# Kernel tuning notes

Measured on AMD Instinct MI355X. Metric: run time of the kernel, lower is better.

The kernel has to match this reference:

```python
import jax, jax.numpy as jnp
import numpy as np

N_NODES = 50000
N_EDGES = 800000
HIDDEN = 128
N_GRAPHS = 256
N_CLASSES = 10


def setup_inputs() -> dict:
    key = jax.random.key(0)
    ks = jax.random.split(key, 9)
    x = jax.random.normal(ks[0], (N_NODES, HIDDEN), dtype=jnp.float32)
    edge_index = jax.random.randint(ks[1], (2, N_EDGES), 0, N_NODES, dtype=jnp.int64)
    batch = jnp.sort(jax.random.randint(ks[2], (N_NODES,), 0, N_GRAPHS, dtype=jnp.int64))
    s = 1.0 / np.sqrt(HIDDEN)
    W1 = jax.random.uniform(ks[3], (HIDDEN, HIDDEN), jnp.float32, -s, s)
    b1 = jax.random.uniform(ks[4], (HIDDEN,), jnp.float32, -s, s)
    W2 = jax.random.uniform(ks[5], (HIDDEN, HIDDEN), jnp.float32, -s, s)
    b2 = jax.random.uniform(ks[6], (HIDDEN,), jnp.float32, -s, s)
    Wl = jax.random.uniform(ks[7], (HIDDEN, N_CLASSES), jnp.float32, -s, s)
    bl = jax.random.uniform(ks[8], (N_CLASSES,), jnp.float32, -s, s)
    return {"x": x, "edge_index": edge_index, "batch": batch,
            "W1": W1, "b1": b1, "W2": W2, "b2": b2, "Wl": Wl, "bl": bl}


def _gin_conv(x, src, dst, W1, b1, W2, b2):
    # GINConv, eps=0: nn(x + sum_{j->i} x_j); messages flow src -> dst
    agg = jax.ops.segment_sum(x[src], dst, num_segments=N_NODES)
    h = x + agg
    h = jnp.maximum(h @ W1 + b1, 0.0) @ W2 + b2  # shared 2-layer MLP
    return h


def reference(x, edge_index, batch, W1, b1, W2, b2, Wl, bl):
    src, dst = edge_index[0], edge_index[1]
    h = jnp.maximum(_gin_conv(x, src, dst, W1, b1, W2, b2), 0.0)
    h = jnp.maximum(_gin_conv(h, src, dst, W1, b1, W2, b2), 0.0)
    h = _gin_conv(h, src, dst, W1, b1, W2, b2)
    # global mean pool over graphs
    sums = jax.ops.segment_sum(h, batch, num_segments=N_GRAPHS)
    cnt = jax.ops.segment_sum(jnp.ones((N_NODES,), h.dtype), batch, num_segments=N_GRAPHS)
    pooled = sums / jnp.maximum(cnt, 1.0)[:, None]
    # dropout is identity in eval mode
    return pooled @ Wl + bl
```

## Files before the change

kernel.cpp:

```cpp
#include <hip/hip_runtime.h>

#define N_NODES  50000
#define N_EDGES  800000
#define HIDDEN   128
#define N_GRAPHS 256
#define N_CLASSES 10
#define WLD 136

typedef short short8 __attribute__((ext_vector_type(8)));
typedef float floatx4 __attribute__((ext_vector_type(4)));

__device__ inline unsigned short bf16_rtne(float x) {
    unsigned u = __float_as_uint(x);
    unsigned r = ((u >> 16) & 1u) + 0x7fffu;
    return (unsigned short)((u + r) >> 16);
}

__global__ void prep_kernel(const int* __restrict__ dst, int* __restrict__ deg, int* __restrict__ epos,
                            const float* __restrict__ W1, unsigned short* __restrict__ W1b,
                            const float* __restrict__ W2, unsigned short* __restrict__ W2b,
                            const float4* __restrict__ X, uint4* __restrict__ Xb,
                            int* __restrict__ counter) {
    int b = blockIdx.x;
    if (b < 3125) {
        int e = b * 256 + threadIdx.x;
        epos[e] = atomicAdd(&deg[dst[e]], 1);
    } else if (b < 3253) {
        int idx = (b - 3125) * 256 + threadIdx.x;
        if (idx == 0) counter[0] = 0;
        int which = idx >> 14, sub = idx & (HIDDEN * HIDDEN - 1);
        int k = sub >> 7, n = sub & 127;
        (which ? W2b : W1b)[n * HIDDEN + k] = bf16_rtne((which ? W2 : W1)[sub]);
    } else {
        int i = (b - 3253) * 256 + threadIdx.x;
        int n = i >> 4, c = i & 15;
        float4 a = X[(size_t)n * 32 + c * 2], v = X[(size_t)n * 32 + c * 2 + 1];
        uint4 o;
        o.x = (unsigned)bf16_rtne(a.x) | ((unsigned)bf16_rtne(a.y) << 16);
        o.y = (unsigned)bf16_rtne(a.z) | ((unsigned)bf16_rtne(a.w) << 16);
        o.z = (unsigned)bf16_rtne(v.x) | ((unsigned)bf16_rtne(v.y) << 16);
        o.w = (unsigned)bf16_rtne(v.z) | ((unsigned)bf16_rtne(v.w) << 16);
        Xb[(size_t)(c >> 2) * N_NODES * 4 + (size_t)n * 4 + (c & 3)] = o;
    }
}

__global__ void offsets_kernel(const int* __restrict__ deg, int* __restrict__ row_start,
                               int* __restrict__ counter) {
    int n = blockIdx.x * blockDim.x + threadIdx.x;
    int d = (n < N_NODES) ? deg[n] : 0;
    int lane = threadIdx.x & 63;
    int incl = d;
    #pragma unroll
    for (int off = 1; off < 64; off <<= 1) {
        int v = __shfl_up(incl, off, 64);
        if (lane >= off) incl += v;
    }
    int excl = incl - d;
    int total = __shfl(incl, 63, 64);
    int base = 0;
    if (lane == 0) base = atomicAdd(counter, total);
    base = __shfl(base, 0, 64);
    if (n < N_NODES) row_start[n] = base + excl;
}

__global__ void place_kernel(const int* __restrict__ src, const int* __restrict__ dst,
                             const int* __restrict__ epos, const int* __restrict__ row_start,
                             int* __restrict__ csr_src) {
    int e = blockIdx.x * blockDim.x + threadIdx.x;
    if (e >= N_EDGES) return;
    csr_src[row_start[dst[e]] + epos[e]] = src[e];
}

__device__ inline void acc_bf2(unsigned d, float& f0, float& f1) {
    f0 += __uint_as_float(d << 16);
    f1 += __uint_as_float(d & 0xffff0000u);
}
__device__ inline void acc8(const uint4 v, float* a) {
    acc_bf2(v.x, a[0], a[1]); acc_bf2(v.y, a[2], a[3]);
    acc_bf2(v.z, a[4], a[5]); acc_bf2(v.w, a[6], a[7]);
}

__global__ void agg_kernel(const uint4* __restrict__ Xb, const int* __restrict__ row_start,
                           const int* __restrict__ deg, const int* __restrict__ csr_src,
                           uint4* __restrict__ Tb ) {
    int s = blockIdx.x & 3;
    int n = (blockIdx.x >> 2) * 64 + (threadIdx.x >> 2);
    int chunk = threadIdx.x & 3;
    if (n >= N_NODES) return;
    const uint4* Ts = Xb + (size_t)s * (N_NODES * 4);
    float a[8];
    #pragma unroll
    for (int j = 0; j < 8; ++j) a[j] = 0.f;
    {
        uint4 v = Ts[(size_t)n * 4 + chunk];
        acc8(v, a);
    }
    int rs = row_start[n], d = deg[n];
    int i = 0;
    for (; i + 8 <= d; i += 8) {
        int s0 = csr_src[rs + i + 0];
        int s1 = csr_src[rs + i + 1];
        int s2 = csr_src[rs + i + 2];
        int s3 = csr_src[rs + i + 3];
        int s4 = csr_src[rs + i + 4];
        int s5 = csr_src[rs + i + 5];
        int s6 = csr_src[rs + i + 6];
        int s7 = csr_src[rs + i + 7];
        uint4 v0 = Ts[(size_t)s0 * 4 + chunk];
        uint4 v1 = Ts[(size_t)s1 * 4 + chunk];
        uint4 v2 = Ts[(size_t)s2 * 4 + chunk];
        uint4 v3 = Ts[(size_t)s3 * 4 + chunk];
        uint4 v4 = Ts[(size_t)s4 * 4 + chunk];
        uint4 v5 = Ts[(size_t)s5 * 4 + chunk];
        uint4 v6 = Ts[(size_t)s6 * 4 + chunk];
        uint4 v7 = Ts[(size_t)s7 * 4 + chunk];
        acc8(v0, a); acc8(v1, a); acc8(v2, a); acc8(v3, a);
        acc8(v4, a); acc8(v5, a); acc8(v6, a); acc8(v7, a);
    }
    for (; i + 2 <= d; i += 2) {
        int s0 = csr_src[rs + i + 0];
        int s1 = csr_src[rs + i + 1];
        uint4 v0 = Ts[(size_t)s0 * 4 + chunk];
        uint4 v1 = Ts[(size_t)s1 * 4 + chunk];
        acc8(v0, a); acc8(v1, a);
    }
    if (i < d) {
        int s0 = csr_src[rs + i];
        uint4 v0 = Ts[(size_t)s0 * 4 + chunk];
        acc8(v0, a);
    }
    uint4 o;
    o.x = (unsigned)bf16_rtne(a[0]) | ((unsigned)bf16_rtne(a[1]) << 16);
    o.y = (unsigned)bf16_rtne(a[2]) | ((unsigned)bf16_rtne(a[3]) << 16);
    o.z = (unsigned)bf16_rtne(a[4]) | ((unsigned)bf16_rtne(a[5]) << 16);
    o.w = (unsigned)bf16_rtne(a[6]) | ((unsigned)bf16_rtne(a[7]) << 16);
    Tb[(size_t)n * 16 + s * 4 + chunk] = o;
}

__global__ __launch_bounds__(256)
void mm_mfma(const unsigned short* __restrict__ Ab,
             const unsigned short* __restrict__ Bw,
             const float* __restrict__ bias,
             unsigned short* __restrict__ Cb, int relu, int blocked) {
    __shared__ unsigned short WhS[64 * WLD];

    int t = threadIdx.x;
    int col_base = blockIdx.y * 64;
    {
        const short8* gh = (const short8*)(Bw + (size_t)col_base * HIDDEN);
        #pragma unroll
        for (int i = 0; i < 4; ++i) {
            int idx = i * 256 + t;
            int row = idx >> 4, kk = (idx & 15) * 8;
            *(short8*)(WhS + row * WLD + kk) = gh[idx];
        }
    }
    __syncthreads();

    int w = t >> 6;
    int l = t & 63;
    int lane16 = l & 15;
    int quad = l >> 4;
    int row_base = blockIdx.x * 128 + w * 32;

    floatx4 acc[2][4];
    #pragma unroll
    for (int m = 0; m < 2; ++m)
        #pragma unroll
        for (int nt = 0; nt < 4; ++nt) acc[m][nt] = (floatx4){0.f, 0.f, 0.f, 0.f};

    #pragma unroll
    for (int kc = 0; kc < 4; ++kc) {
        int k0 = kc * 32 + quad * 8;
        short8 af[2];
        #pragma unroll
        for (int m = 0; m < 2; ++m) {
            int r = row_base + m * 16 + lane16;
            if (r < N_NODES) af[m] = *(const short8*)(Ab + (size_t)r * HIDDEN + k0);
            else             af[m] = (short8){0,0,0,0,0,0,0,0};
        }
        short8 bh[4];
        #pragma unroll
        for (int nt = 0; nt < 4; ++nt)
            bh[nt] = *(const short8*)(WhS + (nt * 16 + lane16) * WLD + k0);
        #pragma unroll
        for (int m = 0; m < 2; ++m)
            #pragma unroll
            for (int nt = 0; nt < 4; ++nt)
                acc[m][nt] = __builtin_amdgcn_mfma_f32_16x16x32_bf16(af[m], bh[nt], acc[m][nt], 0, 0, 0);
    }
    #pragma unroll
    for (int nt = 0; nt < 4; ++nt) {
        int col = col_base + nt * 16 + lane16;
        float b = bias[col];
        #pragma unroll
        for (int m = 0; m < 2; ++m) {
            #pragma unroll
            for (int reg = 0; reg < 4; ++reg) {
                int r = row_base + m * 16 + quad * 4 + reg;
                if (r < N_NODES) {
                    float o = acc[m][nt][reg] + b;
                    if (relu) o = fmaxf(o, 0.f);
                    size_t oi = blocked
                        ? ((size_t)(col >> 5) * N_NODES + r) * 32 + (col & 31)
                        : (size_t)r * HIDDEN + col;
                    Cb[oi] = bf16_rtne(o);
                }
            }
        }
    }
}

__global__ void pool_head_kernel(const unsigned short* __restrict__ H, const int* __restrict__ batch,
                                 const float* __restrict__ Wl, const float* __restrict__ bl,
                                 float* __restrict__ out) {
    int g = blockIdx.x;
    int t = threadIdx.x;
    __shared__ int bounds[2];
    __shared__ float acc2[2 * HIDDEN];
    __shared__ float mean[HIDDEN];

    if (t < 2) {
        int target = g + t;
        int lo = 0, hi = N_NODES;
        while (lo < hi) {
            int mid = (lo + hi) >> 1;
            if (batch[mid] < target) lo = mid + 1; else hi = mid;
        }
        bounds[t] = lo;
    }
    __syncthreads();
    int r0 = bounds[0], r1 = bounds[1];

    int c = t & 127, half = t >> 7;
    float s = 0.f;
    for (int r = r0 + half; r < r1; r += 2)
        s += __uint_as_float((unsigned)H[(size_t)r * HIDDEN + c] << 16);
    acc2[half * HIDDEN + c] = s;
    __syncthreads();
    if (t < HIDDEN) {
        float cntf = (float)(r1 - r0);
        mean[t] = (acc2[t] + acc2[HIDDEN + t]) / fmaxf(cntf, 1.0f);
    }
    __syncthreads();
    if (t < N_CLASSES) {
        float o = bl[t];
        #pragma unroll 8
        for (int k = 0; k < HIDDEN; ++k) o = fmaf(mean[k], Wl[k * N_CLASSES + t], o);
        out[(size_t)g * N_CLASSES + t] = o;
    }
}

extern "C" void kernel_launch(void* const* d_in, const int* in_sizes, int n_in,
                              void* d_out, int out_size, void* d_ws, size_t ws_size,
                              hipStream_t stream) {
    const float* x   = (const float*)d_in[0];
    const int*   ei  = (const int*)d_in[1];
    const int*   bat = (const int*)d_in[2];
    const float* W1  = (const float*)d_in[3];
    const float* b1  = (const float*)d_in[4];
    const float* W2  = (const float*)d_in[5];
    const float* b2  = (const float*)d_in[6];
    const float* Wl  = (const float*)d_in[7];
    const float* bl  = (const float*)d_in[8];
    float* out = (float*)d_out;

    const int* src = ei;
    const int* dst = ei + N_EDGES;

    char* w = (char*)d_ws;
    size_t off = 0;
    auto alloc = [&](size_t bytes) { void* p = w + off; off = (off + bytes + 255) & ~(size_t)255; return p; };
    unsigned short* g_bf  = (unsigned short*)alloc((size_t)N_NODES * HIDDEN * 2);
    unsigned short* t_bf  = (unsigned short*)alloc((size_t)N_NODES * HIDDEN * 2);
    unsigned short* z_bf  = (unsigned short*)alloc((size_t)N_NODES * HIDDEN * 2);
    int*   deg     = (int*)  alloc((size_t)N_NODES * 4);
    int*   rowst   = (int*)  alloc((size_t)N_NODES * 4);
    int*   epos    = (int*)  alloc((size_t)N_EDGES * 4);
    int*   csr_src = (int*)  alloc((size_t)N_EDGES * 4);
    int*   counter = (int*)  alloc(256);
    unsigned short* w1b = (unsigned short*)alloc((size_t)HIDDEN * HIDDEN * 2);
    unsigned short* w2b = (unsigned short*)alloc((size_t)HIDDEN * HIDDEN * 2);
    (void)ws_size; (void)in_sizes; (void)n_in; (void)out_size;

    hipMemsetAsync(deg, 0, (size_t)N_NODES * 4, stream);

    prep_kernel<<<6378, 256, 0, stream>>>(dst, deg, epos, W1, w1b, W2, w2b,
                                          (const float4*)x, (uint4*)g_bf, counter);
    offsets_kernel<<<(N_NODES + 255) / 256, 256, 0, stream>>>(deg, rowst, counter);
    place_kernel<<<(N_EDGES + 255) / 256, 256, 0, stream>>>(src, dst, epos, rowst, csr_src);

    const int agg_grid = 4 * ((N_NODES + 63) / 64);
    const dim3 mm_grid((N_NODES + 127) / 128, 2);

    agg_kernel<<<agg_grid, 256, 0, stream>>>((const uint4*)g_bf, rowst, deg, csr_src, (uint4*)t_bf);
    mm_mfma<<<mm_grid, 256, 0, stream>>>(t_bf, w1b, b1, z_bf, 1, 0);
    mm_mfma<<<mm_grid, 256, 0, stream>>>(z_bf, w2b, b2, g_bf, 1, 1);
    agg_kernel<<<agg_grid, 256, 0, stream>>>((const uint4*)g_bf, rowst, deg, csr_src, (uint4*)t_bf);
    mm_mfma<<<mm_grid, 256, 0, stream>>>(t_bf, w1b, b1, z_bf, 1, 0);
    mm_mfma<<<mm_grid, 256, 0, stream>>>(z_bf, w2b, b2, g_bf, 1, 1);
    agg_kernel<<<agg_grid, 256, 0, stream>>>((const uint4*)g_bf, rowst, deg, csr_src, (uint4*)t_bf);
    mm_mfma<<<mm_grid, 256, 0, stream>>>(t_bf, w1b, b1, z_bf, 1, 0);
    mm_mfma<<<mm_grid, 256, 0, stream>>>(z_bf, w2b, b2, t_bf, 0, 0);

    pool_head_kernel<<<N_GRAPHS, 256, 0, stream>>>(t_bf, bat, Wl, bl, out);
}
```

Measured before the change: 344.5 us.

## Fuse whole GIN pipeline into one cooperative persistent kernel with grid syncs

Replaces the chain of about fourteen kernel launches (memset, CSR build, three agg/MLP layers, pooling) with a single cooperative persistent kernel that loops over work tiles and separates phases with grid.sync(). This is meant to remove per-launch overhead and inter-kernel gaps. The price is a grid capped at 4 blocks per CU, grid-wide barrier costs, and a smaller agg unroll (4 instead of 8). If the cooperative launch fails, it falls back to the multi-kernel path.

```diff
diff --git a/kernel.cpp b/kernel.cpp
--- a/kernel.cpp
+++ b/kernel.cpp
@@ -1,4 +1,7 @@
 #include <hip/hip_runtime.h>
+#include <hip/hip_cooperative_groups.h>
+
+namespace cg = cooperative_groups;
 
 #define N_NODES  50000
 #define N_EDGES  800000
@@ -14,6 +17,238 @@
     unsigned u = __float_as_uint(x);
     unsigned r = ((u >> 16) & 1u) + 0x7fffu;
     return (unsigned short)((u + r) >> 16);
+}
+
+__device__ inline void acc_bf2(unsigned d, float& f0, float& f1) {
+    f0 += __uint_as_float(d << 16);
+    f1 += __uint_as_float(d & 0xffff0000u);
+}
+__device__ inline void acc8(const uint4 v, float* a) {
+    acc_bf2(v.x, a[0], a[1]); acc_bf2(v.y, a[2], a[3]);
+    acc_bf2(v.z, a[4], a[5]); acc_bf2(v.w, a[6], a[7]);
+}
+
+__device__ __forceinline__ void mm_phase(const unsigned short* Ab, const unsigned short* Bw,
+                                         const float* bias, unsigned short* Cb,
+                                         int relu, int blocked,
+                                         unsigned short* WhS, int bid, int nb, int t) {
+    int col_base = (bid & 1) * 64;
+    __syncthreads();
+    {
+        const short8* gh = (const short8*)(Bw + (size_t)col_base * HIDDEN);
+        #pragma unroll
+        for (int i = 0; i < 4; ++i) {
+            int idx = i * 256 + t;
+            int row = idx >> 4, kk = (idx & 15) * 8;
+            *(short8*)(WhS + row * WLD + kk) = gh[idx];
+        }
+    }
+    __syncthreads();
+    int w = t >> 6, l = t & 63;
+    int lane16 = l & 15, quad = l >> 4;
+    for (int tile = bid; tile < 782; tile += nb) {
+        int row_base = (tile >> 1) * 128 + w * 32;
+        floatx4 acc[2][4];
+        #pragma unroll
+        for (int m = 0; m < 2; ++m)
+            #pragma unroll
+            for (int nt = 0; nt < 4; ++nt) acc[m][nt] = (floatx4){0.f, 0.f, 0.f, 0.f};
+        #pragma unroll
+        for (int kc = 0; kc < 4; ++kc) {
+            int k0 = kc * 32 + quad * 8;
+            short8 af[2];
+            #pragma unroll
+            for (int m = 0; m < 2; ++m) {
+                int r = row_base + m * 16 + lane16;
+                if (r < N_NODES) af[m] = *(const short8*)(Ab + (size_t)r * HIDDEN + k0);
+                else             af[m] = (short8){0,0,0,0,0,0,0,0};
+            }
+            short8 bh[4];
+            #pragma unroll
+            for (int nt = 0; nt < 4; ++nt)
+                bh[nt] = *(const short8*)(WhS + (nt * 16 + lane16) * WLD + k0);
+            #pragma unroll
+            for (int m = 0; m < 2; ++m)
+                #pragma unroll
+                for (int nt = 0; nt < 4; ++nt)
+                    acc[m][nt] = __builtin_amdgcn_mfma_f32_16x16x32_bf16(af[m], bh[nt], acc[m][nt], 0, 0, 0);
+        }
+        #pragma unroll
+        for (int nt = 0; nt < 4; ++nt) {
+            int col = col_base + nt * 16 + lane16;
+            float b = bias[col];
+            #pragma unroll
+            for (int m = 0; m < 2; ++m) {
+                #pragma unroll
+                for (int reg = 0; reg < 4; ++reg) {
+                    int r = row_base + m * 16 + quad * 4 + reg;
+                    if (r < N_NODES) {
+                        float o = acc[m][nt][reg] + b;
+                        if (relu) o = fmaxf(o, 0.f);
+                        size_t oi = blocked
+                            ? ((size_t)(col >> 5) * N_NODES + r) * 32 + (col & 31)
+                            : (size_t)r * HIDDEN + col;
+                        Cb[oi] = bf16_rtne(o);
+                    }
+                }
+            }
+        }
+    }
+}
+
+__device__ __forceinline__ void agg_tile(const unsigned short* g_bf, const int* row_start,
+                                         const int* deg, const int* csr_src,
+                                         unsigned short* t_bf, int tile, int t) {
+    int s = tile & 3;
+    int n = (tile >> 2) * 64 + (t >> 2);
+    int chunk = t & 3;
+    if (n < N_NODES) {
+        const uint4* Ts = (const uint4*)g_bf + (size_t)s * (N_NODES * 4);
+        float a[8];
+        #pragma unroll
+        for (int j = 0; j < 8; ++j) a[j] = 0.f;
+        {
+            uint4 v = Ts[(size_t)n * 4 + chunk];
+            acc8(v, a);
+        }
+        int rs = row_start[n], d = deg[n];
+        int i = 0;
+        for (; i + 4 <= d; i += 4) {
+            int s0 = csr_src[rs + i + 0];
+            int s1 = csr_src[rs + i + 1];
+            int s2 = csr_src[rs + i + 2];
+            int s3 = csr_src[rs + i + 3];
+            uint4 v0 = Ts[(size_t)s0 * 4 + chunk];
+            uint4 v1 = Ts[(size_t)s1 * 4 + chunk];
+            uint4 v2 = Ts[(size_t)s2 * 4 + chunk];
+            uint4 v3 = Ts[(size_t)s3 * 4 + chunk];
+            acc8(v0, a); acc8(v1, a); acc8(v2, a); acc8(v3, a);
+        }
+        for (; i < d; ++i) {
+            int s0 = csr_src[rs + i];
+            uint4 v0 = Ts[(size_t)s0 * 4 + chunk];
+            acc8(v0, a);
+        }
+        uint4 o;
+        o.x = (unsigned)bf16_rtne(a[0]) | ((unsigned)bf16_rtne(a[1]) << 16);
+        o.y = (unsigned)bf16_rtne(a[2]) | ((unsigned)bf16_rtne(a[3]) << 16);
+        o.z = (unsigned)bf16_rtne(a[4]) | ((unsigned)bf16_rtne(a[5]) << 16);
+        o.w = (unsigned)bf16_rtne(a[6]) | ((unsigned)bf16_rtne(a[7]) << 16);
+        ((uint4*)t_bf)[(size_t)n * 16 + s * 4 + chunk] = o;
+    }
+}
+
+__global__ __launch_bounds__(256, 4)
+void mega_kernel(const int* src, const int* dst, int* deg, int* epos, int* rowst,
+                 int* csr_src, int* counter,
+                 const float* W1, const float* W2,
+                 unsigned short* w1b, unsigned short* w2b,
+                 const float* b1, const float* b2,
+                 const float4* X, unsigned short* g_bf, unsigned short* t_bf,
+                 unsigned short* z_bf,
+                 const int* batch, const float* Wl, const float* bl, float* out) {
+    cg::grid_group grid = cg::this_grid();
+    const int nb = gridDim.x;
+    const int bid = blockIdx.x;
+    const int t = threadIdx.x;
+
+    __shared__ unsigned short WhS[64 * WLD];
+    __shared__ int bounds[2];
+    __shared__ float pacc[2 * HIDDEN];
+    __shared__ float pmean[HIDDEN];
+
+    for (int i = bid * 256 + t; i < N_NODES; i += nb * 256) deg[i] = 0;
+    if (bid == 0 && t == 0) counter[0] = 0;
+    grid.sync();
+
+    for (int b = bid; b < 6378; b += nb) {
+        if (b < 3125) {
+            int e = b * 256 + t;
+            epos[e] = atomicAdd(&deg[dst[e]], 1);
+        } else if (b < 3253) {
+            int idx = (b - 3125) * 256 + t;
+            int which = idx >> 14, sub = idx & (HIDDEN * HIDDEN - 1);
+            int k = sub >> 7, n = sub & 127;
+            (which ? w2b : w1b)[n * HIDDEN + k] = bf16_rtne((which ? W2 : W1)[sub]);
+        } else {
+            int i = (b - 3253) * 256 + t;
+            int n = i >> 4, c = i & 15;
+            float4 a = X[(size_t)n * 32 + c * 2], v = X[(size_t)n * 32 + c * 2 + 1];
+            uint4 o;
+            o.x = (unsigned)bf16_rtne(a.x) | ((unsigned)bf16_rtne(a.y) << 16);
+            o.y = (unsigned)bf16_rtne(a.z) | ((unsigned)bf16_rtne(a.w) << 16);
+            o.z = (unsigned)bf16_rtne(v.x) | ((unsigned)bf16_rtne(v.y) << 16);
+            o.w = (unsigned)bf16_rtne(v.z) | ((unsigned)bf16_rtne(v.w) << 16);
+            ((uint4*)g_bf)[(size_t)(c >> 2) * N_NODES * 4 + (size_t)n * 4 + (c & 3)] = o;
+        }
+    }
+    grid.sync();
+
+    for (int base = bid * 256; base < N_NODES; base += nb * 256) {
+        int n = base + t;
+        int d = (n < N_NODES) ? deg[n] : 0;
+        int lane = t & 63;
+        int incl = d;
+        #pragma unroll
+        for (int o = 1; o < 64; o <<= 1) {
+            int v = __shfl_up(incl, o, 64);
+            if (lane >= o) incl += v;
+        }
+        int excl = incl - d;
+        int total = __shfl(incl, 63, 64);
+        int bse = 0;
+        if (lane == 0) bse = atomicAdd(counter, total);
+        bse = __shfl(bse, 0, 64);
+        if (n < N_NODES) rowst[n] = bse + excl;
+    }
+    grid.sync();
+
+    for (int e = bid * 256 + t; e < N_EDGES; e += nb * 256)
+        csr_src[rowst[dst[e]] + epos[e]] = src[e];
+    grid.sync();
+
+    for (int layer = 0; layer < 3; ++layer) {
+        for (int tile = bid; tile < 3128; tile += nb)
+            agg_tile(g_bf, rowst, deg, csr_src, t_bf, tile, t);
+        grid.sync();
+        mm_phase(t_bf, w1b, b1, z_bf, 1, 0, WhS, bid, nb, t);
+        grid.sync();
+        if (layer < 2) mm_phase(z_bf, w2b, b2, g_bf, 1, 1, WhS, bid, nb, t);
+        else           mm_phase(z_bf, w2b, b2, t_bf, 0, 0, WhS, bid, nb, t);
+        grid.sync();
+    }
+
+    for (int g = bid; g < N_GRAPHS; g += nb) {
+        __syncthreads();
+        if (t < 2) {
+            int target = g + t;
+            int lo = 0, hi = N_NODES;
+            while (lo < hi) {
+                int mid = (lo + hi) >> 1;
+                if (batch[mid] < target) lo = mid + 1; else hi = mid;
+            }
+            bounds[t] = lo;
+        }
+        __syncthreads();
+        int r0 = bounds[0], r1 = bounds[1];
+        int c = t & 127, half = t >> 7;
+        float s = 0.f;
+        for (int r = r0 + half; r < r1; r += 2)
+            s += __uint_as_float((unsigned)t_bf[(size_t)r * HIDDEN + c] << 16);
+        pacc[half * HIDDEN + c] = s;
+        __syncthreads();
+        if (t < HIDDEN) {
+            float cntf = (float)(r1 - r0);
+            pmean[t] = (pacc[t] + pacc[HIDDEN + t]) / fmaxf(cntf, 1.0f);
+        }
+        __syncthreads();
+        if (t < N_CLASSES) {
+            float o = bl[t];
+            #pragma unroll 8
+            for (int k = 0; k < HIDDEN; ++k) o = fmaf(pmean[k], Wl[k * N_CLASSES + t], o);
+            out[(size_t)g * N_CLASSES + t] = o;
+        }
+    }
 }
 
 __global__ void prep_kernel(const int* __restrict__ dst, int* __restrict__ deg, int* __restrict__ epos,
@@ -51,9 +286,9 @@
     int lane = threadIdx.x & 63;
     int incl = d;
     #pragma unroll
-    for (int off = 1; off < 64; off <<= 1) {
-        int v = __shfl_up(incl, off, 64);
-        if (lane >= off) incl += v;
+    for (int o = 1; o < 64; o <<= 1) {
+        int v = __shfl_up(incl, o, 64);
+        if (lane >= o) incl += v;
     }
     int excl = incl - d;
     int total = __shfl(incl, 63, 64);
@@ -71,144 +306,19 @@
     csr_src[row_start[dst[e]] + epos[e]] = src[e];
 }
 
-__device__ inline void acc_bf2(unsigned d, float& f0, float& f1) {
-    f0 += __uint_as_float(d << 16);
-    f1 += __uint_as_float(d & 0xffff0000u);
-}
-__device__ inline void acc8(const uint4 v, float* a) {
-    acc_bf2(v.x, a[0], a[1]); acc_bf2(v.y, a[2], a[3]);
-    acc_bf2(v.z, a[4], a[5]); acc_bf2(v.w, a[6], a[7]);
-}
-
-__global__ void agg_kernel(const uint4* __restrict__ Xb, const int* __restrict__ row_start,
+__global__ void agg_kernel(const unsigned short* __restrict__ Xb, const int* __restrict__ row_start,
                            const int* __restrict__ deg, const int* __restrict__ csr_src,
-                           uint4* __restrict__ Tb ) {
-    int s = blockIdx.x & 3;
-    int n = (blockIdx.x >> 2) * 64 + (threadIdx.x >> 2);
-    int chunk = threadIdx.x & 3;
-    if (n >= N_NODES) return;
-    const uint4* Ts = Xb + (size_t)s * (N_NODES * 4);
-    float a[8];
-    #pragma unroll
-    for (int j = 0; j < 8; ++j) a[j] = 0.f;
-    {
-        uint4 v = Ts[(size_t)n * 4 + chunk];
-        acc8(v, a);
-    }
-    int rs = row_start[n], d = deg[n];
-    int i = 0;
-    for (; i + 8 <= d; i += 8) {
-        int s0 = csr_src[rs + i + 0];
-        int s1 = csr_src[rs + i + 1];
-        int s2 = csr_src[rs + i + 2];
-        int s3 = csr_src[rs + i + 3];
-        int s4 = csr_src[rs + i + 4];
-        int s5 = csr_src[rs + i + 5];
-        int s6 = csr_src[rs + i + 6];
-        int s7 = csr_src[rs + i + 7];
-        uint4 v0 = Ts[(size_t)s0 * 4 + chunk];
-        uint4 v1 = Ts[(size_t)s1 * 4 + chunk];
-        uint4 v2 = Ts[(size_t)s2 * 4 + chunk];
-        uint4 v3 = Ts[(size_t)s3 * 4 + chunk];
-        uint4 v4 = Ts[(size_t)s4 * 4 + chunk];
-        uint4 v5 = Ts[(size_t)s5 * 4 + chunk];
-        uint4 v6 = Ts[(size_t)s6 * 4 + chunk];
-        uint4 v7 = Ts[(size_t)s7 * 4 + chunk];
-        acc8(v0, a); acc8(v1, a); acc8(v2, a); acc8(v3, a);
-        acc8(v4, a); acc8(v5, a); acc8(v6, a); acc8(v7, a);
-    }
-    for (; i + 2 <= d; i += 2) {
-        int s0 = csr_src[rs + i + 0];
-        int s1 = csr_src[rs + i + 1];
-        uint4 v0 = Ts[(size_t)s0 * 4 + chunk];
-        uint4 v1 = Ts[(size_t)s1 * 4 + chunk];
-        acc8(v0, a); acc8(v1, a);
-    }
-    if (i < d) {
-        int s0 = csr_src[rs + i];
-        uint4 v0 = Ts[(size_t)s0 * 4 + chunk];
-        acc8(v0, a);
-    }
-    uint4 o;
-    o.x = (unsigned)bf16_rtne(a[0]) | ((unsigned)bf16_rtne(a[1]) << 16);
-    o.y = (unsigned)bf16_rtne(a[2]) | ((unsigned)bf16_rtne(a[3]) << 16);
-    o.z = (unsigned)bf16_rtne(a[4]) | ((unsigned)bf16_rtne(a[5]) << 16);
-    o.w = (unsigned)bf16_rtne(a[6]) | ((unsigned)bf16_rtne(a[7]) << 16);
-    Tb[(size_t)n * 16 + s * 4 + chunk] = o;
+                           unsigned short* __restrict__ Tb) {
+    agg_tile(Xb, row_start, deg, csr_src, Tb, blockIdx.x, threadIdx.x);
 }
 
 __global__ __launch_bounds__(256)
-void mm_mfma(const unsigned short* __restrict__ Ab,
-             const unsigned short* __restrict__ Bw,
-             const float* __restrict__ bias,
-             unsigned short* __restrict__ Cb, int relu, int blocked) {
+void mm_kernel(const unsigned short* __restrict__ Ab, const unsigned short* __restrict__ Bw,
+               const float* __restrict__ bias, unsigned short* __restrict__ Cb,
+               int relu, int blocked) {
     __shared__ unsigned short WhS[64 * WLD];
-
-    int t = threadIdx.x;
-    int col_base = blockIdx.y * 64;
-    {
-        const short8* gh = (const short8*)(Bw + (size_t)col_base * HIDDEN);
-        #pragma unroll
-        for (int i = 0; i < 4; ++i) {
-            int idx = i * 256 + t;
-            int row = idx >> 4, kk = (idx & 15) * 8;
-            *(short8*)(WhS + row * WLD + kk) = gh[idx];
-        }
-    }
-    __syncthreads();
-
-    int w = t >> 6;
-    int l = t & 63;
-    int lane16 = l & 15;
-    int quad = l >> 4;
-    int row_base = blockIdx.x * 128 + w * 32;
-
-    floatx4 acc[2][4];
-    #pragma unroll
-    for (int m = 0; m < 2; ++m)
-        #pragma unroll
-        for (int nt = 0; nt < 4; ++nt) acc[m][nt] = (floatx4){0.f, 0.f, 0.f, 0.f};
-
-    #pragma unroll
-    for (int kc = 0; kc < 4; ++kc) {
-        int k0 = kc * 32 + quad * 8;
-        short8 af[2];
-        #pragma unroll
-        for (int m = 0; m < 2; ++m) {
-            int r = row_base + m * 16 + lane16;
-            if (r < N_NODES) af[m] = *(const short8*)(Ab + (size_t)r * HIDDEN + k0);
-            else             af[m] = (short8){0,0,0,0,0,0,0,0};
-        }
-        short8 bh[4];
-        #pragma unroll
-        for (int nt = 0; nt < 4; ++nt)
-            bh[nt] = *(const short8*)(WhS + (nt * 16 + lane16) * WLD + k0);
-        #pragma unroll
-        for (int m = 0; m < 2; ++m)
-            #pragma unroll
-            for (int nt = 0; nt < 4; ++nt)
-                acc[m][nt] = __builtin_amdgcn_mfma_f32_16x16x32_bf16(af[m], bh[nt], acc[m][nt], 0, 0, 0);
-    }
-    #pragma unroll
-    for (int nt = 0; nt < 4; ++nt) {
-        int col = col_base + nt * 16 + lane16;
-        float b = bias[col];
-        #pragma unroll
-        for (int m = 0; m < 2; ++m) {
-            #pragma unroll
-            for (int reg = 0; reg < 4; ++reg) {
-                int r = row_base + m * 16 + quad * 4 + reg;
-                if (r < N_NODES) {
-                    float o = acc[m][nt][reg] + b;
-                    if (relu) o = fmaxf(o, 0.f);
-                    size_t oi = blocked
-                        ? ((size_t)(col >> 5) * N_NODES + r) * 32 + (col & 31)
-                        : (size_t)r * HIDDEN + col;
-                    Cb[oi] = bf16_rtne(o);
-                }
-            }
-        }
-    }
+    int bid = blockIdx.x;
+    mm_phase(Ab, Bw, bias, Cb, relu, blocked, WhS, bid, 782, threadIdx.x);
 }
 
 __global__ void pool_head_kernel(const unsigned short* __restrict__ H, const int* __restrict__ batch,
@@ -219,7 +329,6 @@
     __shared__ int bounds[2];
     __shared__ float acc2[2 * HIDDEN];
     __shared__ float mean[HIDDEN];
-
     if (t < 2) {
         int target = g + t;
         int lo = 0, hi = N_NODES;
@@ -231,7 +340,6 @@
     }
     __syncthreads();
     int r0 = bounds[0], r1 = bounds[1];
-
     int c = t & 127, half = t >> 7;
     float s = 0.f;
     for (int r = r0 + half; r < r1; r += 2)
@@ -267,6 +375,7 @@
 
     const int* src = ei;
     const int* dst = ei + N_EDGES;
+    const float4* x4 = (const float4*)x;
 
     char* w = (char*)d_ws;
     size_t off = 0;
@@ -283,25 +392,30 @@
     unsigned short* w2b = (unsigned short*)alloc((size_t)HIDDEN * HIDDEN * 2);
     (void)ws_size; (void)in_sizes; (void)n_in; (void)out_size;
 
-    hipMemsetAsync(deg, 0, (size_t)N_NODES * 4, stream);
-
-    prep_kernel<<<6378, 256, 0, stream>>>(dst, deg, epos, W1, w1b, W2, w2b,
-                                          (const float4*)x, (uint4*)g_bf, counter);
-    offsets_kernel<<<(N_NODES + 255) / 256, 256, 0, stream>>>(deg, rowst, counter);
-    place_kernel<<<(N_EDGES + 255) / 256, 256, 0, stream>>>(src, dst, epos, rowst, csr_src);
-
-    const int agg_grid = 4 * ((N_NODES + 63) / 64);
-    const dim3 mm_grid((N_NODES + 127) / 128, 2);
-
-    agg_kernel<<<agg_grid, 256, 0, stream>>>((const uint4*)g_bf, rowst, deg, csr_src, (uint4*)t_bf);
-    mm_mfma<<<mm_grid, 256, 0, stream>>>(t_bf, w1b, b1, z_bf, 1, 0);
-    mm_mfma<<<mm_grid, 256, 0, stream>>>(z_bf, w2b, b2, g_bf, 1, 1);
-    agg_kernel<<<agg_grid, 256, 0, stream>>>((const uint4*)g_bf, rowst, deg, csr_src, (uint4*)t_bf);
-    mm_mfma<<<mm_grid, 256, 0, stream>>>(t_bf, w1b, b1, z_bf, 1, 0);
-    mm_mfma<<<mm_grid, 256, 0, stream>>>(z_bf, w2b, b2, g_bf, 1, 1);
-    agg_kernel<<<agg_grid, 256, 0, stream>>>((const uint4*)g_bf, rowst, deg, csr_src, (uint4*)t_bf);
-    mm_mfma<<<mm_grid, 256, 0, stream>>>(t_bf, w1b, b1, z_bf, 1, 0);
-    mm_mfma<<<mm_grid, 256, 0, stream>>>(z_bf, w2b, b2, t_bf, 0, 0);
-
-    pool_head_kernel<<<N_GRAPHS, 256, 0, stream>>>(t_bf, bat, Wl, bl, out);
-}
+    int maxB = 0;
+    hipOccupancyMaxActiveBlocksPerMultiprocessor(&maxB, mega_kernel, 256, 0);
+    if (maxB < 1) maxB = 1;
+    if (maxB > 4) maxB = 4;
+    int grid = maxB * 256;
+
+    void* args[] = { &src, &dst, &deg, &epos, &rowst, &csr_src, &counter,
+                     &W1, &W2, &w1b, &w2b, &b1, &b2, &x4, &g_bf, &t_bf, &z_bf,
+                     &bat, &Wl, &bl, &out };
+    hipError_t err = hipLaunchCooperativeKernel((void*)mega_kernel, dim3(grid), dim3(256),
+                                                args, 0, stream);
+    if (err != hipSuccess) {
+        hipMemsetAsync(deg, 0, (size_t)N_NODES * 4, stream);
+        prep_kernel<<<6378, 256, 0, stream>>>(dst, deg, epos, W1, w1b, W2, w2b,
+                                              x4, (uint4*)g_bf, counter);
+        offsets_kernel<<<(N_NODES + 255) / 256, 256, 0, stream>>>(deg, rowst, counter);
+        place_kernel<<<(N_EDGES + 255) / 256, 256, 0, stream>>>(src, dst, epos, rowst, csr_src);
+        const int agg_grid = 4 * ((N_NODES + 63) / 64);
+        for (int layer = 0; layer < 3; ++layer) {
+            agg_kernel<<<agg_grid, 256, 0, stream>>>(g_bf, rowst, deg, csr_src, t_bf);
+            mm_kernel<<<782, 256, 0, stream>>>(t_bf, w1b, b1, z_bf, 1, 0);
+            if (layer < 2) mm_kernel<<<782, 256, 0, stream>>>(z_bf, w2b, b2, g_bf, 1, 1);
+            else           mm_kernel<<<782, 256, 0, stream>>>(z_bf, w2b, b2, t_bf, 0, 0);
+        }
+        pool_head_kernel<<<N_GRAPHS, 256, 0, stream>>>(t_bf, bat, Wl, bl, out);
+    }
+}
```

Result: slower. 1.217 ms (+253.2%).
